# Performance work log

Hardware: AMD Instinct MI355X
Metric: run time of the kernel (lower is better)

Reference implementation:

```python
import jax, jax.numpy as jnp
import numpy as np

# GNB per-element parameters [s, beta, R, C6] indexed by atomic number Z (rows not listed stay zero)
_ROWS = {
 1:[0.2772,1.7504,3.6516,95.99], 2:[0.2425,2.087,2.1843,40.67], 3:[0.3266,2.3073,1.2711,70.21],
 4:[0.3964,2.8811,3.3497,114.51], 5:[0.3121,2.6366,2.7079,152.36], 6:[0.2455,3.0189,1.8219,184.28],
 7:[0.2743,2.9432,2.4667,482.54], 8:[0.2577,2.7407,2.365,405.57], 9:[0.2791,2.5863,1.5062,218.45],
 10:[0.2378,2.5307,1.8233,174.81], 11:[0.2592,2.5679,1.3974,181.7], 12:[0.3837,2.9613,3.3515,263.02],
 13:[0.3013,3.2377,3.0102,228.1], 14:[0.3202,3.2749,3.1629,359.43], 15:[0.3399,3.7491,3.2554,3222.12],
 16:[0.3215,3.6718,2.9539,2144.49], 17:[0.3071,3.418,3.0368,2072.46], 18:[0.2752,3.3306,2.6598,1357.42],
 19:[0.2264,2.9736,4.0877,1406.65], 20:[0.4015,3.4464,4.1275,1058.36], 21:[0.9388,4.5955,9.7282,11498.73],
 22:[0.6048,3.5334,8.5322,3361.33], 23:[0.3678,3.068,7.2344,2095.91], 24:[0.2848,2.8393,5.3605,1049.31],
 25:[0.355,3.055,3.718,966.27], 26:[0.4406,3.2628,3.6408,1571.36], 27:[0.4124,3.2622,3.4961,1183.59],
 28:[0.3139,2.749,3.5108,787.76], 29:[0.3345,2.9097,3.0537,563.93], 30:[0.3391,2.9024,3.0261,592.91],
 31:[0.3146,3.3924,3.1735,430.82], 32:[0.3327,3.2804,3.1773,812.57], 33:[0.404,3.8757,3.8357,4533.53],
 34:[0.3343,3.8562,3.1109,3440.92], 35:[0.3242,3.7067,3.2122,3859.82], 36:[0.292,3.6457,2.8263,2729.6],
 37:[0.2677,3.4421,2.412,1864.19], 38:[0.3446,3.559,1.894,1175.73], 39:[1.0038,5.7293,11.2061,32141.18],
 40:[0.6146,5.075,6.821,27655.14], 41:[0.4244,3.7156,7.2367,2864.2], 42:[0.4882,3.6853,3.901,3563.45],
 43:[0.4439,3.6987,4.0857,3266.43], 44:[0.4736,3.7826,4.045,3967.23], 45:[0.4039,3.4706,3.4813,2233.82],
 46:[0.3188,3.3433,3.0487,1393.49], 47:[0.2948,3.1186,2.7795,1315.09], 48:[0.3012,3.0853,2.8673,1311.47],
 49:[0.3351,3.5452,3.3339,1460.56], 50:[0.3134,3.2997,3.0086,1662.99], 51:[0.4081,4.1277,3.9919,8089.97],
 52:[0.3585,4.1795,3.4209,6887.05], 53:[0.3574,4.0988,3.5649,8799.32], 54:[0.3134,4.0387,3.0288,6136.5],
 55:[0.2872,3.8468,2.262,3757.31], 56:[0.3788,4.0368,1.3837,2561.18], 57:[1.0851,6.1365,12.171,66580.83],
 72:[0.5577,5.213,6.0791,27593.76], 73:[0.5308,4.7637,5.7661,15364.65], 74:[0.3926,3.6018,3.6366,2734.5],
 75:[0.5351,3.9552,4.241,4801.82], 76:[0.4701,4.0278,4.1348,5685.94], 77:[0.3661,3.6123,3.4213,2786.0],
 78:[0.3411,3.6066,3.2486,2699.79], 79:[0.3164,3.3822,2.9588,2282.6], 80:[0.3047,3.375,2.9381,2476.79],
 81:[0.2802,3.3964,2.7711,2988.7], 82:[0.2682,3.2481,2.5816,2506.63], 83:[0.3876,4.1225,3.785,8916.84],
 84:[0.3679,4.2313,3.5381,8694.22], 85:[0.368,4.2455,3.6985,11821.61], 86:[0.3195,4.1784,3.0551,8410.64],
}
_TAB = np.zeros((87, 4), np.float32)
for _z, _v in _ROWS.items():
    _TAB[_z] = _v
GNB_TABLE = jnp.asarray(_TAB)
C_SP2 = jnp.asarray(np.array([0.2808, 3.0548, 2.2348, 429.69], np.float32))
C_SP3 = jnp.asarray(np.array([0.2455, 3.0189, 1.8219, 184.28], np.float32))
N_CN2 = jnp.asarray(np.array([0.2996, 3.02, 2.6454, 720.18], np.float32))
N_CN3 = jnp.asarray(np.array([0.2743, 2.9432, 2.4667, 482.54], np.float32))

BJ_A1, BJ_A2, BJ_ALPHA = 0.4, 4.0, 14.0
CUTOFF_LR, CUTOFF_START = 10.0, 8.0  # cutoff_start = cutoff_lr - 2.0


def _poly_envelope(x):
    # PolynomialCutoff.calculate_envelope with r_max=1, p=6:
    x6 = x ** 6
    env = 1.0 - 28.0 * x6 + 48.0 * x6 * x - 21.0 * x6 * x * x
    return env * (x < 1.0)


def _gnb_forward(lengths, Z, edge_index):
    n_nodes = Z.shape[0]
    sender, receiver = edge_index[0], edge_index[1]

    # coordination numbers via scatter-add on receiver
    cn = jnp.zeros((n_nodes,), jnp.int32).at[receiver].add(1)

    # species-indexed params with CN-adaptive selection for C and N
    params = GNB_TABLE[Z]  # [N, 4]
    c_params = jnp.where((cn <= 3)[:, None], C_SP2[None, :], C_SP3[None, :])
    n_params = jnp.where((cn <= 2)[:, None], N_CN2[None, :], N_CN3[None, :])
    params = jnp.where((Z == 6)[:, None], c_params, params)
    params = jnp.where((Z == 7)[:, None], n_params, params)

    R_i = params[:, 2]
    C6_i = params[:, 3]

    # geometric-mean combination rules per edge
    C6_ij = jnp.sqrt(C6_i[sender] * C6_i[receiver])
    R_ij = jnp.sqrt(R_i[sender] * R_i[receiver])

    r = lengths
    # BJ damping: f = 1 / (1 + 6 (r/r0)^(-alpha)), r0 = a1 sqrt(R_ij) + a2
    r0 = BJ_A1 * jnp.sqrt(R_ij) + BJ_A2
    f_damp = 1.0 / (1.0 + 6.0 * (r0 / r) ** BJ_ALPHA)

    e_edge = -C6_ij / (R_ij ** 6 + r ** 6) * f_damp

    # long-range polynomial cutoff switching from 1 at cutoff_start to 0 at cutoff_lr
    x = (r - CUTOFF_START) / (CUTOFF_LR - CUTOFF_START)
    env = jnp.where(r < CUTOFF_START, 1.0, _poly_envelope(x))
    e_edge = e_edge * env

    # scatter-sum to atoms; 0.5 to split symmetric pair energy over both directions
    node_energy = jnp.zeros((n_nodes,), e_edge.dtype).at[receiver].add(0.5 * e_edge)
    return node_energy


def setup_inputs() -> dict:
    key = jax.random.key(0)
    k1, k2, k3 = jax.random.split(key, 3)
    n_nodes, n_edges = 100000, 6400000
    Z = jax.random.randint(k1, (n_nodes,), 1, 87, dtype=jnp.int32)
    edge_index = jax.random.randint(k2, (2, n_edges), 0, n_nodes, dtype=jnp.int32)
    lengths = jax.random.uniform(k3, (n_edges,), jnp.float32, 1.0, 10.5)
    return {"Z": Z, "edge_index": edge_index, "lengths": lengths}


def reference(Z, edge_index, lengths):
    return _gnb_forward(lengths, Z, edge_index)
```

## Files before the change

### kernel.cpp

```cpp
#include <hip/hip_runtime.h>


#define B2SHIFT 10
#define B2SIZE  1024
#define TILE    4096
#define SBLK    512
#define ESLICES 8
#define MAXB    128
#define AREP    4

__device__ __constant__ float2 GNB_RC6[87] = {
    {0.f, 0.f},
    {3.6516f, 95.99f},   {2.1843f, 40.67f},   {1.2711f, 70.21f},
    {3.3497f, 114.51f},  {2.7079f, 152.36f},  {1.8219f, 184.28f},
    {2.4667f, 482.54f},  {2.365f, 405.57f},   {1.5062f, 218.45f},
    {1.8233f, 174.81f},  {1.3974f, 181.7f},   {3.3515f, 263.02f},
    {3.0102f, 228.1f},   {3.1629f, 359.43f},  {3.2554f, 3222.12f},
    {2.9539f, 2144.49f}, {3.0368f, 2072.46f}, {2.6598f, 1357.42f},
    {4.0877f, 1406.65f}, {4.1275f, 1058.36f}, {9.7282f, 11498.73f},
    {8.5322f, 3361.33f}, {7.2344f, 2095.91f}, {5.3605f, 1049.31f},
    {3.718f, 966.27f},   {3.6408f, 1571.36f}, {3.4961f, 1183.59f},
    {3.5108f, 787.76f},  {3.0537f, 563.93f},  {3.0261f, 592.91f},
    {3.1735f, 430.82f},  {3.1773f, 812.57f},  {3.8357f, 4533.53f},
    {3.1109f, 3440.92f}, {3.2122f, 3859.82f}, {2.8263f, 2729.6f},
    {2.412f, 1864.19f},  {1.894f, 1175.73f},  {11.2061f, 32141.18f},
    {6.821f, 27655.14f}, {7.2367f, 2864.2f},  {3.901f, 3563.45f},
    {4.0857f, 3266.43f}, {4.045f, 3967.23f},  {3.4813f, 2233.82f},
    {3.0487f, 1393.49f}, {2.7795f, 1315.09f}, {2.8673f, 1311.47f},
    {3.3339f, 1460.56f}, {3.0086f, 1662.99f}, {3.9919f, 8089.97f},
    {3.4209f, 6887.05f}, {3.5649f, 8799.32f}, {3.0288f, 6136.5f},
    {2.262f, 3757.31f},  {1.3837f, 2561.18f}, {12.171f, 66580.83f},
    {0.f,0.f},{0.f,0.f},{0.f,0.f},{0.f,0.f},{0.f,0.f},{0.f,0.f},{0.f,0.f},
    {0.f,0.f},{0.f,0.f},{0.f,0.f},{0.f,0.f},{0.f,0.f},{0.f,0.f},{0.f,0.f},
    {6.0791f, 27593.76f}, {5.7661f, 15364.65f}, {3.6366f, 2734.5f},
    {4.241f, 4801.82f},   {4.1348f, 5685.94f},  {3.4213f, 2786.0f},
    {3.2486f, 2699.79f},  {2.9588f, 2282.6f},   {2.9381f, 2476.79f},
    {2.7711f, 2988.7f},   {2.5816f, 2506.63f},  {3.785f, 8916.84f},
    {3.5381f, 8694.22f},  {3.6985f, 11821.61f}, {3.0551f, 8410.64f},
};

__global__ void gnb_init(const int* __restrict__ Z, unsigned* __restrict__ isCN,
                         int nw, int n_nodes, int4* __restrict__ zp4, int zq,
                         int* __restrict__ zp, int zwords) {
    int stride = gridDim.x * blockDim.x;
    int t0 = blockIdx.x * blockDim.x + threadIdx.x;
    int4 z4 = make_int4(0, 0, 0, 0);
    for (int i = t0; i < zq; i += stride) zp4[i] = z4;
    for (int i = zq * 4 + t0; i < zwords; i += stride) zp[i] = 0;
    for (int w = t0; w < nw; w += stride) {
        unsigned m = 0;
        int base = w << 5;
        int lim = n_nodes - base; if (lim > 32) lim = 32;
        for (int k = 0; k < lim; ++k) {
            int z = Z[base + k];
            if (z == 6 || z == 7) m |= (1u << k);
        }
        isCN[w] = m;
    }
}

__global__ void gnb_params(const int* __restrict__ Z, const int* __restrict__ cn,
                           float2* __restrict__ P2, int n_nodes) {
    int i = blockIdx.x * blockDim.x + threadIdx.x;
    if (i >= n_nodes) return;
    int z = Z[i];
    float Rp, C6;
    if (z == 6) {
        if (cn[i] <= 3) { Rp = 2.2348f; C6 = 429.69f; }
        else            { Rp = 1.8219f; C6 = 184.28f; }
    } else if (z == 7) {
        if (cn[i] <= 2) { Rp = 2.6454f; C6 = 720.18f; }
        else            { Rp = 2.4667f; C6 = 482.54f; }
    } else {
        float2 rc = GNB_RC6[z];
        Rp = rc.x; C6 = rc.y;
    }
    P2[i] = make_float2(sqrtf(C6), sqrtf(sqrtf(Rp)));
}

__device__ __forceinline__ float gnb_energy_eval(float2 ps, float2 pr, float rlen) {
    float env;
    if (rlen < 8.0f) {
        env = 1.0f;
    } else {
        float x = (rlen - 8.0f) * 0.5f;
        float x2 = x * x;
        float x6 = x2 * x2 * x2;
        env = 1.0f - 28.0f * x6 + 48.0f * x6 * x - 21.0f * x6 * x2;
    }
    float sR  = ps.y * pr.y;
    float C6  = ps.x * pr.x;
    float Rij = sR * sR;
    float R3  = Rij * Rij * Rij;
    float R6  = R3 * R3;
    float r0  = 0.4f * sR + 4.0f;
    float t   = r0 / rlen;
    float t2 = t * t, t4 = t2 * t2, t8 = t4 * t4;
    float t14 = t8 * t4 * t2;
    float fd = 1.0f / (1.0f + 6.0f * t14);
    float rl2 = rlen * rlen;
    float r6 = rl2 * rl2 * rl2;
    return -0.5f * C6 / (R6 + r6) * fd * env;
}

__global__ void __launch_bounds__(SBLK)
gnb_scatter(const int* __restrict__ send, const int* __restrict__ recv,
            const float* __restrict__ len, const unsigned* __restrict__ isCN,
            int* __restrict__ cn,
            uint2* __restrict__ buckets, unsigned* __restrict__ cursor,
            uint4* __restrict__ ovrec, unsigned* __restrict__ ocur,
            int n_edges, unsigned cap, unsigned ocap) {
    __shared__ unsigned hist[MAXB];
    __shared__ unsigned gbase[MAXB];
    const int tid = threadIdx.x;
    const int e0  = blockIdx.x * TILE;

    if (tid < MAXB) hist[tid] = 0;
    __syncthreads();

    unsigned ss[8]; unsigned rr[8]; float ll[8];
    const bool full = (e0 + TILE <= n_edges);
    if (full) {
        int4   sv0 = *(const int4*)(send + e0 + tid * 4);
        int4   rv0 = *(const int4*)(recv + e0 + tid * 4);
        float4 lv0 = *(const float4*)(len + e0 + tid * 4);
        int4   sv1 = *(const int4*)(send + e0 + 2048 + tid * 4);
        int4   rv1 = *(const int4*)(recv + e0 + 2048 + tid * 4);
        float4 lv1 = *(const float4*)(len + e0 + 2048 + tid * 4);
        ss[0]=(unsigned)sv0.x; ss[1]=(unsigned)sv0.y; ss[2]=(unsigned)sv0.z; ss[3]=(unsigned)sv0.w;
        ss[4]=(unsigned)sv1.x; ss[5]=(unsigned)sv1.y; ss[6]=(unsigned)sv1.z; ss[7]=(unsigned)sv1.w;
        rr[0]=(unsigned)rv0.x; rr[1]=(unsigned)rv0.y; rr[2]=(unsigned)rv0.z; rr[3]=(unsigned)rv0.w;
        rr[4]=(unsigned)rv1.x; rr[5]=(unsigned)rv1.y; rr[6]=(unsigned)rv1.z; rr[7]=(unsigned)rv1.w;
        ll[0]=lv0.x; ll[1]=lv0.y; ll[2]=lv0.z; ll[3]=lv0.w;
        ll[4]=lv1.x; ll[5]=lv1.y; ll[6]=lv1.z; ll[7]=lv1.w;
    } else {
        #pragma unroll
        for (int i = 0; i < 8; ++i) {
            int e = e0 + ((i >> 2) * 2048) + tid * 4 + (i & 3);
            bool ok = (e < n_edges);
            ss[i] = ok ? (unsigned)send[e] : 0u;
            rr[i] = ok ? (unsigned)recv[e] : 0u;
            ll[i] = ok ? len[e] : 1.0e9f;
        }
    }

    #pragma unroll
    for (int i = 0; i < 8; ++i) {
        if (ll[i] < 1.0e8f && ((isCN[rr[i] >> 5] >> (rr[i] & 31)) & 1u))
            atomicAdd(&cn[rr[i]], 1);
    }

    unsigned bk[8];
    #pragma unroll
    for (int i = 0; i < 8; ++i) {
        if (ll[i] < 10.0f) {
            unsigned b   = rr[i] >> B2SHIFT;
            unsigned off = atomicAdd(&hist[b], 1u);
            bk[i] = b | (off << 7);
        } else {
            bk[i] = 0x80000000u;
        }
    }
    __syncthreads();

    if (tid < MAXB) {
        unsigned c = hist[tid];
        gbase[tid] = c ? atomicAdd(&cursor[tid], c) : 0u;
    }
    __syncthreads();

    #pragma unroll
    for (int i = 0; i < 8; ++i) {
        unsigned bo = bk[i];
        if (!(bo & 0x80000000u)) {
            unsigned b = bo & (MAXB - 1);
            unsigned g = gbase[b] + (bo >> 7);
            unsigned x = ss[i] | ((rr[i] & (B2SIZE - 1)) << 17);
            if (g < cap) {
                buckets[(size_t)b * cap + g] = make_uint2(x, __float_as_uint(ll[i]));
            } else {
                unsigned o = atomicAdd(ocur, 1u);
                if (o < ocap)
                    ovrec[o] = make_uint4(rr[i], ss[i], __float_as_uint(ll[i]), 0u);
            }
        }
    }
}

__global__ void __launch_bounds__(256)
gnb_accum(const uint2* __restrict__ buckets, const unsigned* __restrict__ cursor,
          const uint4* __restrict__ ovrec, const unsigned* __restrict__ ocur,
          const float2* __restrict__ P2, float* __restrict__ rep,
          unsigned cap, unsigned ocap, int n_nodes) {
    __shared__ float  acc[AREP][B2SIZE + 8];
    __shared__ float2 p2loc[B2SIZE];
    const int b   = blockIdx.x / ESLICES;
    const int sl  = blockIdx.x % ESLICES;
    const int tid = threadIdx.x;
    const int rp  = (tid >> 6) & (AREP - 1);

    for (int i = tid; i < AREP * (B2SIZE + 8); i += 256) acc[0][i] = 0.0f;
    for (int i = tid; i < B2SIZE; i += 256) {
        int node = (b << B2SHIFT) + i;
        p2loc[i] = (node < n_nodes) ? P2[node] : make_float2(0.f, 0.f);
    }
    __syncthreads();

    unsigned count = cursor[b];
    if (count > cap) count = cap;
    unsigned seg = (((count + ESLICES - 1) / ESLICES) + 3u) & ~3u;
    unsigned st  = (unsigned)sl * seg; if (st > count) st = count;
    unsigned en  = st + seg; if (en > count) en = count;

    const uint2* src = buckets + (size_t)b * cap;
    for (unsigned i = st + tid * 4; i < en; i += 1024) {
        if (i + 4 <= en) {
            uint4 q0 = *(const uint4*)(src + i);
            uint4 q1 = *(const uint4*)(src + i + 2);
            unsigned sx[4] = {q0.x, q0.z, q1.x, q1.z};
            unsigned lb[4] = {q0.y, q0.w, q1.y, q1.w};
            float2 ps[4];
            #pragma unroll
            for (int j = 0; j < 4; ++j) ps[j] = P2[sx[j] & 0x1FFFFu];
            #pragma unroll
            for (int j = 0; j < 4; ++j) {
                unsigned rlow = (sx[j] >> 17) & (B2SIZE - 1);
                float e = gnb_energy_eval(ps[j], p2loc[rlow], __uint_as_float(lb[j]));
                atomicAdd(&acc[rp][rlow], e);
            }
        } else {
            for (unsigned t = i; t < en; ++t) {
                uint2 rec = src[t];
                unsigned rlow = (rec.x >> 17) & (B2SIZE - 1);
                float e = gnb_energy_eval(P2[rec.x & 0x1FFFFu], p2loc[rlow],
                                          __uint_as_float(rec.y));
                atomicAdd(&acc[rp][rlow], e);
            }
        }
    }

    if (sl == 0) {
        unsigned n = *ocur; if (n > ocap) n = ocap;
        for (unsigned i = tid; i < n; i += 256) {
            uint4 rc = ovrec[i];
            if ((rc.x >> B2SHIFT) == (unsigned)b) {
                float e = gnb_energy_eval(P2[rc.y], p2loc[rc.x & (B2SIZE - 1)],
                                          __uint_as_float(rc.z));
                atomicAdd(&acc[rp][rc.x & (B2SIZE - 1)], e);
            }
        }
    }
    __syncthreads();

    float* dst = rep + (size_t)blockIdx.x * B2SIZE;
    for (int i = tid; i < B2SIZE; i += 256)
        dst[i] = (acc[0][i] + acc[1][i]) + (acc[2][i] + acc[3][i]);
}

__global__ void gnb_reduce(const float* __restrict__ rep, float* __restrict__ out,
                           int n_nodes) {
    int i = blockIdx.x * blockDim.x + threadIdx.x;
    if (i >= n_nodes) return;
    int b = i >> B2SHIFT;
    int j = i & (B2SIZE - 1);
    const float* src = rep + ((size_t)b * ESLICES) * B2SIZE + j;
    float sum = 0.0f;
    #pragma unroll
    for (int s = 0; s < ESLICES; ++s) sum += src[(size_t)s * B2SIZE];
    out[i] = sum;
}

extern "C" void kernel_launch(void* const* d_in, const int* in_sizes, int n_in,
                              void* d_out, int out_size, void* d_ws, size_t ws_size,
                              hipStream_t stream) {
    const int*   Z    = (const int*)d_in[0];
    const int*   eidx = (const int*)d_in[1];
    const float* len  = (const float*)d_in[2];
    float*       out  = (float*)d_out;

    const int n_nodes = in_sizes[0];
    const int n_edges = in_sizes[2];
    const int* send = eidx;
    const int* recv = eidx + n_edges;

    const int NB2 = (n_nodes + B2SIZE - 1) >> B2SHIFT;
    const int nw  = (n_nodes + 31) >> 5;
    const int nwp = (nw + 7) & ~7;

    char* ws = (char*)d_ws;
    unsigned* cursor = (unsigned*)ws;
    unsigned* ocur   = (unsigned*)(ws + MAXB * 4);
    int*      cn     = (int*)(ws + (MAXB + 8) * 4);
    float2*   P2     = (float2*)(ws + ((size_t)n_nodes + MAXB + 8) * 4);
    unsigned* isCN   = (unsigned*)(ws + ((size_t)3 * n_nodes + MAXB + 8) * 4);
    float*    rep    = (float*)((char*)isCN + (size_t)nwp * 4);
    size_t rep_w     = (size_t)NB2 * ESLICES * B2SIZE;
    char*     tail   = (char*)rep + rep_w * 4;

    size_t fixed_words = (size_t)3 * n_nodes + MAXB + 8 + nwp + rep_w;
    size_t total_words = ws_size / 4;
    size_t avail = total_words > fixed_words ? total_words - fixed_words : 0;
    size_t ovw = avail / 64;
    unsigned ocap = (unsigned)(ovw / 4);
    size_t capw = (avail - ovw) / (size_t)NB2;
    long cap = (long)((capw / 2) & ~(size_t)3);
    if (cap > n_edges) cap = (n_edges + 3) & ~3;
    if (cap < 0) cap = 0;
    uint4* ovrec   = (uint4*)tail;
    uint2* buckets = (uint2*)(tail + (size_t)ocap * 16);

    const int B = 256;
    int node_blocks = (n_nodes + B - 1) / B;
    int scat_blocks = (n_edges + TILE - 1) / TILE;
    int zero_words  = n_nodes + MAXB + 8;
    int zq = zero_words / 4;

    gnb_init<<<256, B, 0, stream>>>(Z, isCN, nw, n_nodes, (int4*)ws, zq,
                                    (int*)ws, zero_words);
    gnb_scatter<<<scat_blocks, SBLK, 0, stream>>>(send, recv, len, isCN, cn,
                                                  buckets, cursor, ovrec, ocur,
                                                  n_edges, (unsigned)cap, ocap);
    gnb_params<<<node_blocks, B, 0, stream>>>(Z, cn, P2, n_nodes);
    gnb_accum<<<NB2 * ESLICES, B, 0, stream>>>(buckets, cursor, ovrec, ocur,
                                               P2, rep, (unsigned)cap, ocap,
                                               n_nodes);
    gnb_reduce<<<node_blocks, B, 0, stream>>>(rep, out, n_nodes);
}
```

Baseline: 200.0 us.

## Fuse pipeline into single cooperative persistent kernel with work-stealing phases

Replaces the five separate launches (init, scatter, params, accum, reduce) with one cooperative kernel. The kernel separates the phases with grid-wide syncs and uses atomic work-stealing counters to hand out edge tiles and accumulation units. The scatter tile shrinks to 2048 edges per 256-thread block, and accumulation slices per bucket rise from 8 to 32 for better load balance. The aim is to remove launch gaps and tail imbalance. In exchange it pays for grid syncs and reads a larger partial-sum buffer in the final reduction. The original multi-kernel path is kept as a fallback if the cooperative launch fails.

```diff
diff --git a/kernel.cpp b/kernel.cpp
--- a/kernel.cpp
+++ b/kernel.cpp
@@ -1,13 +1,19 @@
 #include <hip/hip_runtime.h>
+#include <hip/hip_cooperative_groups.h>
+
+namespace cg = cooperative_groups;
 
 
 #define B2SHIFT 10
 #define B2SIZE  1024
-#define TILE    4096
-#define SBLK    512
-#define ESLICES 8
 #define MAXB    128
+#define ESLICES 32
+#define BLK     256
+#define EPT     8
+#define STILE   (BLK * EPT)
 #define AREP    4
+#define FTILE   4096
+#define FSBLK   512
 
 __device__ __constant__ float2 GNB_RC6[87] = {
     {0.f, 0.f},
@@ -39,45 +45,6 @@
     {3.5381f, 8694.22f},  {3.6985f, 11821.61f}, {3.0551f, 8410.64f},
 };
 
-__global__ void gnb_init(const int* __restrict__ Z, unsigned* __restrict__ isCN,
-                         int nw, int n_nodes, int4* __restrict__ zp4, int zq,
-                         int* __restrict__ zp, int zwords) {
-    int stride = gridDim.x * blockDim.x;
-    int t0 = blockIdx.x * blockDim.x + threadIdx.x;
-    int4 z4 = make_int4(0, 0, 0, 0);
-    for (int i = t0; i < zq; i += stride) zp4[i] = z4;
-    for (int i = zq * 4 + t0; i < zwords; i += stride) zp[i] = 0;
-    for (int w = t0; w < nw; w += stride) {
-        unsigned m = 0;
-        int base = w << 5;
-        int lim = n_nodes - base; if (lim > 32) lim = 32;
-        for (int k = 0; k < lim; ++k) {
-            int z = Z[base + k];
-            if (z == 6 || z == 7) m |= (1u << k);
-        }
-        isCN[w] = m;
-    }
-}
-
-__global__ void gnb_params(const int* __restrict__ Z, const int* __restrict__ cn,
-                           float2* __restrict__ P2, int n_nodes) {
-    int i = blockIdx.x * blockDim.x + threadIdx.x;
-    if (i >= n_nodes) return;
-    int z = Z[i];
-    float Rp, C6;
-    if (z == 6) {
-        if (cn[i] <= 3) { Rp = 2.2348f; C6 = 429.69f; }
-        else            { Rp = 1.8219f; C6 = 184.28f; }
-    } else if (z == 7) {
-        if (cn[i] <= 2) { Rp = 2.6454f; C6 = 720.18f; }
-        else            { Rp = 2.4667f; C6 = 482.54f; }
-    } else {
-        float2 rc = GNB_RC6[z];
-        Rp = rc.x; C6 = rc.y;
-    }
-    P2[i] = make_float2(sqrtf(C6), sqrtf(sqrtf(Rp)));
-}
-
 __device__ __forceinline__ float gnb_energy_eval(float2 ps, float2 pr, float rlen) {
     float env;
     if (rlen < 8.0f) {
@@ -103,23 +70,277 @@
     return -0.5f * C6 / (R6 + r6) * fd * env;
 }
 
-__global__ void __launch_bounds__(SBLK)
-gnb_scatter(const int* __restrict__ send, const int* __restrict__ recv,
-            const float* __restrict__ len, const unsigned* __restrict__ isCN,
-            int* __restrict__ cn,
-            uint2* __restrict__ buckets, unsigned* __restrict__ cursor,
-            uint4* __restrict__ ovrec, unsigned* __restrict__ ocur,
-            int n_edges, unsigned cap, unsigned ocap) {
+__device__ __forceinline__ void params_one(const int* Z, const int* cn,
+                                           float2* P2, int i) {
+    int z = Z[i];
+    float Rp, C6;
+    if (z == 6) {
+        if (cn[i] <= 3) { Rp = 2.2348f; C6 = 429.69f; }
+        else            { Rp = 1.8219f; C6 = 184.28f; }
+    } else if (z == 7) {
+        if (cn[i] <= 2) { Rp = 2.6454f; C6 = 720.18f; }
+        else            { Rp = 2.4667f; C6 = 482.54f; }
+    } else {
+        float2 rc = GNB_RC6[z];
+        Rp = rc.x; C6 = rc.y;
+    }
+    P2[i] = make_float2(sqrtf(C6), sqrtf(sqrtf(Rp)));
+}
+
+__global__ void __launch_bounds__(BLK)
+gnb_fused(const int* __restrict__ Z, const int* __restrict__ send,
+          const int* __restrict__ recv, const float* __restrict__ len,
+          float* __restrict__ out,
+          unsigned* __restrict__ cursor, unsigned* __restrict__ cntrs,
+          int* __restrict__ cn, float2* __restrict__ P2,
+          unsigned* __restrict__ isCN, float* __restrict__ rep,
+          uint4* __restrict__ ovrec, uint2* __restrict__ buckets,
+          int n_nodes, int n_edges, unsigned cap, unsigned ocap,
+          int nw, int NB2, int ntiles, int nunits) {
+    cg::grid_group grid = cg::this_grid();
+    __shared__ union {
+        struct { unsigned hist[MAXB]; unsigned gbase[MAXB]; } s;
+        struct { float acc[AREP][B2SIZE + 8]; float2 p2loc[B2SIZE]; } a;
+    } sh;
+    __shared__ unsigned steal;
+    const int tid = threadIdx.x;
+    const int gtid = blockIdx.x * BLK + tid;
+    const int gstride = gridDim.x * BLK;
+    unsigned* ocur = cntrs + 0;
+    unsigned* scur = cntrs + 1;
+    unsigned* ucur = cntrs + 2;
+
+    {
+        int zwords = MAXB + 8 + n_nodes;
+        int zq = zwords >> 2;
+        int4* zp4 = (int4*)cursor;
+        int4 z4 = make_int4(0, 0, 0, 0);
+        for (int i = gtid; i < zq; i += gstride) zp4[i] = z4;
+        for (int i = (zq << 2) + gtid; i < zwords; i += gstride)
+            ((int*)cursor)[i] = 0;
+        int nal = (n_nodes + 63) & ~63;
+        for (int i = gtid; i < nal; i += gstride) {
+            bool pred = false;
+            if (i < n_nodes) { int z = Z[i]; pred = (z == 6) | (z == 7); }
+            unsigned long long m = __ballot(pred);
+            if ((tid & 63) == 0) {
+                int w = i >> 5;
+                if (w < nw)     isCN[w]     = (unsigned)m;
+                if (w + 1 < nw) isCN[w + 1] = (unsigned)(m >> 32);
+            }
+        }
+    }
+    grid.sync();
+
+    for (;;) {
+        if (tid == 0) steal = atomicAdd(scur, 1u);
+        __syncthreads();
+        unsigned t = steal;
+        if (t >= (unsigned)ntiles) break;
+        if (tid < MAXB) sh.s.hist[tid] = 0;
+        __syncthreads();
+
+        const int e0 = (int)t * STILE;
+        unsigned ss[EPT]; unsigned rr[EPT]; float ll[EPT];
+        const bool full = (e0 + STILE <= n_edges);
+        if (full) {
+            int4   sv0 = *(const int4*)(send + e0 + tid * 4);
+            int4   rv0 = *(const int4*)(recv + e0 + tid * 4);
+            float4 lv0 = *(const float4*)(len + e0 + tid * 4);
+            int4   sv1 = *(const int4*)(send + e0 + 1024 + tid * 4);
+            int4   rv1 = *(const int4*)(recv + e0 + 1024 + tid * 4);
+            float4 lv1 = *(const float4*)(len + e0 + 1024 + tid * 4);
+            ss[0]=(unsigned)sv0.x; ss[1]=(unsigned)sv0.y; ss[2]=(unsigned)sv0.z; ss[3]=(unsigned)sv0.w;
+            ss[4]=(unsigned)sv1.x; ss[5]=(unsigned)sv1.y; ss[6]=(unsigned)sv1.z; ss[7]=(unsigned)sv1.w;
+            rr[0]=(unsigned)rv0.x; rr[1]=(unsigned)rv0.y; rr[2]=(unsigned)rv0.z; rr[3]=(unsigned)rv0.w;
+            rr[4]=(unsigned)rv1.x; rr[5]=(unsigned)rv1.y; rr[6]=(unsigned)rv1.z; rr[7]=(unsigned)rv1.w;
+            ll[0]=lv0.x; ll[1]=lv0.y; ll[2]=lv0.z; ll[3]=lv0.w;
+            ll[4]=lv1.x; ll[5]=lv1.y; ll[6]=lv1.z; ll[7]=lv1.w;
+        } else {
+            #pragma unroll
+            for (int i = 0; i < EPT; ++i) {
+                int e = e0 + ((i >> 2) * 1024) + tid * 4 + (i & 3);
+                bool ok = (e < n_edges);
+                ss[i] = ok ? (unsigned)send[e] : 0u;
+                rr[i] = ok ? (unsigned)recv[e] : 0u;
+                ll[i] = ok ? len[e] : 1.0e9f;
+            }
+        }
+
+        #pragma unroll
+        for (int i = 0; i < EPT; ++i) {
+            if (ll[i] < 1.0e8f && ((isCN[rr[i] >> 5] >> (rr[i] & 31)) & 1u))
+                atomicAdd(&cn[rr[i]], 1);
+        }
+
+        unsigned bk[EPT];
+        #pragma unroll
+        for (int i = 0; i < EPT; ++i) {
+            if (ll[i] < 10.0f) {
+                unsigned b   = rr[i] >> B2SHIFT;
+                unsigned off = atomicAdd(&sh.s.hist[b], 1u);
+                bk[i] = b | (off << 7);
+            } else {
+                bk[i] = 0x80000000u;
+            }
+        }
+        __syncthreads();
+
+        if (tid < MAXB) {
+            unsigned c = sh.s.hist[tid];
+            sh.s.gbase[tid] = c ? atomicAdd(&cursor[tid], c) : 0u;
+        }
+        __syncthreads();
+
+        #pragma unroll
+        for (int i = 0; i < EPT; ++i) {
+            unsigned bo = bk[i];
+            if (!(bo & 0x80000000u)) {
+                unsigned b = bo & (MAXB - 1);
+                unsigned g = sh.s.gbase[b] + (bo >> 7);
+                unsigned x = ss[i] | ((rr[i] & (B2SIZE - 1)) << 17);
+                if (g < cap) {
+                    buckets[(size_t)b * cap + g] =
+                        make_uint2(x, __float_as_uint(ll[i]));
+                } else {
+                    unsigned o = atomicAdd(ocur, 1u);
+                    if (o < ocap)
+                        ovrec[o] = make_uint4(rr[i], ss[i],
+                                              __float_as_uint(ll[i]), 0u);
+                }
+            }
+        }
+    }
+    grid.sync();
+
+    for (int i = gtid; i < n_nodes; i += gstride) params_one(Z, cn, P2, i);
+    grid.sync();
+
+    for (;;) {
+        if (tid == 0) steal = atomicAdd(ucur, 1u);
+        __syncthreads();
+        unsigned u = steal;
+        if (u >= (unsigned)nunits) break;
+        const int b  = (int)(u >> 5);
+        const int sl = (int)(u & (ESLICES - 1));
+        const int rp = (tid >> 6) & (AREP - 1);
+
+        float* accf = &sh.a.acc[0][0];
+        for (int i = tid; i < AREP * (B2SIZE + 8); i += BLK) accf[i] = 0.0f;
+        for (int i = tid; i < B2SIZE; i += BLK) {
+            int node = (b << B2SHIFT) + i;
+            sh.a.p2loc[i] = (node < n_nodes) ? P2[node] : make_float2(0.f, 0.f);
+        }
+        __syncthreads();
+
+        unsigned count = cursor[b];
+        if (count > cap) count = cap;
+        unsigned seg = (((count + ESLICES - 1) / ESLICES) + 3u) & ~3u;
+        unsigned st  = (unsigned)sl * seg; if (st > count) st = count;
+        unsigned en  = st + seg; if (en > count) en = count;
+
+        const uint2* src = buckets + (size_t)b * cap;
+        for (unsigned i = st + tid * 4; i < en; i += BLK * 4) {
+            if (i + 4 <= en) {
+                uint4 q0 = *(const uint4*)(src + i);
+                uint4 q1 = *(const uint4*)(src + i + 2);
+                unsigned sx[4] = {q0.x, q0.z, q1.x, q1.z};
+                unsigned lb[4] = {q0.y, q0.w, q1.y, q1.w};
+                float2 ps[4];
+                #pragma unroll
+                for (int j = 0; j < 4; ++j) ps[j] = P2[sx[j] & 0x1FFFFu];
+                #pragma unroll
+                for (int j = 0; j < 4; ++j) {
+                    unsigned rlow = (sx[j] >> 17) & (B2SIZE - 1);
+                    float e = gnb_energy_eval(ps[j], sh.a.p2loc[rlow],
+                                              __uint_as_float(lb[j]));
+                    atomicAdd(&sh.a.acc[rp][rlow], e);
+                }
+            } else {
+                for (unsigned q = i; q < en; ++q) {
+                    uint2 rec = src[q];
+                    unsigned rlow = (rec.x >> 17) & (B2SIZE - 1);
+                    float e = gnb_energy_eval(P2[rec.x & 0x1FFFFu],
+                                              sh.a.p2loc[rlow],
+                                              __uint_as_float(rec.y));
+                    atomicAdd(&sh.a.acc[rp][rlow], e);
+                }
+            }
+        }
+
+        if (sl == 0) {
+            unsigned n = *ocur; if (n > ocap) n = ocap;
+            for (unsigned i = tid; i < n; i += BLK) {
+                uint4 rc = ovrec[i];
+                if ((rc.x >> B2SHIFT) == (unsigned)b) {
+                    float e = gnb_energy_eval(P2[rc.y],
+                                              sh.a.p2loc[rc.x & (B2SIZE - 1)],
+                                              __uint_as_float(rc.z));
+                    atomicAdd(&sh.a.acc[rp][rc.x & (B2SIZE - 1)], e);
+                }
+            }
+        }
+        __syncthreads();
+
+        float* dst = rep + (size_t)u * B2SIZE;
+        for (int i = tid; i < B2SIZE; i += BLK)
+            dst[i] = (sh.a.acc[0][i] + sh.a.acc[1][i]) +
+                     (sh.a.acc[2][i] + sh.a.acc[3][i]);
+    }
+    grid.sync();
+
+    for (int i = gtid; i < n_nodes; i += gstride) {
+        int b = i >> B2SHIFT;
+        int j = i & (B2SIZE - 1);
+        const float* src = rep + ((size_t)b * ESLICES) * B2SIZE + j;
+        float s = 0.0f;
+        #pragma unroll
+        for (int k = 0; k < ESLICES; ++k) s += src[(size_t)k * B2SIZE];
+        out[i] = s;
+    }
+}
+
+__global__ void fb_init(const int* __restrict__ Z, unsigned* __restrict__ isCN,
+                        int nw, int n_nodes, int4* __restrict__ zp4, int zq,
+                        int* __restrict__ zp, int zwords) {
+    int stride = gridDim.x * blockDim.x;
+    int t0 = blockIdx.x * blockDim.x + threadIdx.x;
+    int4 z4 = make_int4(0, 0, 0, 0);
+    for (int i = t0; i < zq; i += stride) zp4[i] = z4;
+    for (int i = zq * 4 + t0; i < zwords; i += stride) zp[i] = 0;
+    for (int w = t0; w < nw; w += stride) {
+        unsigned m = 0;
+        int base = w << 5;
+        int lim = n_nodes - base; if (lim > 32) lim = 32;
+        for (int k = 0; k < lim; ++k) {
+            int z = Z[base + k];
+            if (z == 6 || z == 7) m |= (1u << k);
+        }
+        isCN[w] = m;
+    }
+}
+
+__global__ void fb_params(const int* __restrict__ Z, const int* __restrict__ cn,
+                          float2* __restrict__ P2, int n_nodes) {
+    int i = blockIdx.x * blockDim.x + threadIdx.x;
+    if (i < n_nodes) params_one(Z, cn, P2, i);
+}
+
+__global__ void __launch_bounds__(FSBLK)
+fb_scatter(const int* __restrict__ send, const int* __restrict__ recv,
+           const float* __restrict__ len, const unsigned* __restrict__ isCN,
+           int* __restrict__ cn,
+           uint2* __restrict__ buckets, unsigned* __restrict__ cursor,
+           uint4* __restrict__ ovrec, unsigned* __restrict__ ocur,
+           int n_edges, unsigned cap, unsigned ocap) {
     __shared__ unsigned hist[MAXB];
     __shared__ unsigned gbase[MAXB];
     const int tid = threadIdx.x;
-    const int e0  = blockIdx.x * TILE;
-
+    const int e0  = blockIdx.x * FTILE;
     if (tid < MAXB) hist[tid] = 0;
     __syncthreads();
-
     unsigned ss[8]; unsigned rr[8]; float ll[8];
-    const bool full = (e0 + TILE <= n_edges);
+    const bool full = (e0 + FTILE <= n_edges);
     if (full) {
         int4   sv0 = *(const int4*)(send + e0 + tid * 4);
         int4   rv0 = *(const int4*)(recv + e0 + tid * 4);
@@ -143,13 +364,11 @@
             ll[i] = ok ? len[e] : 1.0e9f;
         }
     }
-
     #pragma unroll
     for (int i = 0; i < 8; ++i) {
         if (ll[i] < 1.0e8f && ((isCN[rr[i] >> 5] >> (rr[i] & 31)) & 1u))
             atomicAdd(&cn[rr[i]], 1);
     }
-
     unsigned bk[8];
     #pragma unroll
     for (int i = 0; i < 8; ++i) {
@@ -162,13 +381,11 @@
         }
     }
     __syncthreads();
-
     if (tid < MAXB) {
         unsigned c = hist[tid];
         gbase[tid] = c ? atomicAdd(&cursor[tid], c) : 0u;
     }
     __syncthreads();
-
     #pragma unroll
     for (int i = 0; i < 8; ++i) {
         unsigned bo = bk[i];
@@ -187,33 +404,30 @@
     }
 }
 
-__global__ void __launch_bounds__(256)
-gnb_accum(const uint2* __restrict__ buckets, const unsigned* __restrict__ cursor,
-          const uint4* __restrict__ ovrec, const unsigned* __restrict__ ocur,
-          const float2* __restrict__ P2, float* __restrict__ rep,
-          unsigned cap, unsigned ocap, int n_nodes) {
+__global__ void __launch_bounds__(BLK)
+fb_accum(const uint2* __restrict__ buckets, const unsigned* __restrict__ cursor,
+         const uint4* __restrict__ ovrec, const unsigned* __restrict__ ocur,
+         const float2* __restrict__ P2, float* __restrict__ rep,
+         unsigned cap, unsigned ocap, int n_nodes) {
     __shared__ float  acc[AREP][B2SIZE + 8];
     __shared__ float2 p2loc[B2SIZE];
     const int b   = blockIdx.x / ESLICES;
     const int sl  = blockIdx.x % ESLICES;
     const int tid = threadIdx.x;
     const int rp  = (tid >> 6) & (AREP - 1);
-
-    for (int i = tid; i < AREP * (B2SIZE + 8); i += 256) acc[0][i] = 0.0f;
-    for (int i = tid; i < B2SIZE; i += 256) {
+    for (int i = tid; i < AREP * (B2SIZE + 8); i += BLK) acc[0][i] = 0.0f;
+    for (int i = tid; i < B2SIZE; i += BLK) {
         int node = (b << B2SHIFT) + i;
         p2loc[i] = (node < n_nodes) ? P2[node] : make_float2(0.f, 0.f);
     }
     __syncthreads();
-
     unsigned count = cursor[b];
     if (count > cap) count = cap;
     unsigned seg = (((count + ESLICES - 1) / ESLICES) + 3u) & ~3u;
     unsigned st  = (unsigned)sl * seg; if (st > count) st = count;
     unsigned en  = st + seg; if (en > count) en = count;
-
     const uint2* src = buckets + (size_t)b * cap;
-    for (unsigned i = st + tid * 4; i < en; i += 1024) {
+    for (unsigned i = st + tid * 4; i < en; i += BLK * 4) {
         if (i + 4 <= en) {
             uint4 q0 = *(const uint4*)(src + i);
             uint4 q1 = *(const uint4*)(src + i + 2);
@@ -229,8 +443,8 @@
                 atomicAdd(&acc[rp][rlow], e);
             }
         } else {
-            for (unsigned t = i; t < en; ++t) {
-                uint2 rec = src[t];
+            for (unsigned q = i; q < en; ++q) {
+                uint2 rec = src[q];
                 unsigned rlow = (rec.x >> 17) & (B2SIZE - 1);
                 float e = gnb_energy_eval(P2[rec.x & 0x1FFFFu], p2loc[rlow],
                                           __uint_as_float(rec.y));
@@ -238,10 +452,9 @@
             }
         }
     }
-
     if (sl == 0) {
         unsigned n = *ocur; if (n > ocap) n = ocap;
-        for (unsigned i = tid; i < n; i += 256) {
+        for (unsigned i = tid; i < n; i += BLK) {
             uint4 rc = ovrec[i];
             if ((rc.x >> B2SHIFT) == (unsigned)b) {
                 float e = gnb_energy_eval(P2[rc.y], p2loc[rc.x & (B2SIZE - 1)],
@@ -251,14 +464,13 @@
         }
     }
     __syncthreads();
-
     float* dst = rep + (size_t)blockIdx.x * B2SIZE;
-    for (int i = tid; i < B2SIZE; i += 256)
+    for (int i = tid; i < B2SIZE; i += BLK)
         dst[i] = (acc[0][i] + acc[1][i]) + (acc[2][i] + acc[3][i]);
 }
 
-__global__ void gnb_reduce(const float* __restrict__ rep, float* __restrict__ out,
-                           int n_nodes) {
+__global__ void fb_reduce(const float* __restrict__ rep, float* __restrict__ out,
+                          int n_nodes) {
     int i = blockIdx.x * blockDim.x + threadIdx.x;
     if (i >= n_nodes) return;
     int b = i >> B2SHIFT;
@@ -289,7 +501,7 @@
 
     char* ws = (char*)d_ws;
     unsigned* cursor = (unsigned*)ws;
-    unsigned* ocur   = (unsigned*)(ws + MAXB * 4);
+    unsigned* cntrs  = (unsigned*)(ws + MAXB * 4);
     int*      cn     = (int*)(ws + (MAXB + 8) * 4);
     float2*   P2     = (float2*)(ws + ((size_t)n_nodes + MAXB + 8) * 4);
     unsigned* isCN   = (unsigned*)(ws + ((size_t)3 * n_nodes + MAXB + 8) * 4);
@@ -309,20 +521,51 @@
     uint4* ovrec   = (uint4*)tail;
     uint2* buckets = (uint2*)(tail + (size_t)ocap * 16);
 
-    const int B = 256;
-    int node_blocks = (n_nodes + B - 1) / B;
-    int scat_blocks = (n_edges + TILE - 1) / TILE;
-    int zero_words  = n_nodes + MAXB + 8;
-    int zq = zero_words / 4;
-
-    gnb_init<<<256, B, 0, stream>>>(Z, isCN, nw, n_nodes, (int4*)ws, zq,
-                                    (int*)ws, zero_words);
-    gnb_scatter<<<scat_blocks, SBLK, 0, stream>>>(send, recv, len, isCN, cn,
-                                                  buckets, cursor, ovrec, ocur,
-                                                  n_edges, (unsigned)cap, ocap);
-    gnb_params<<<node_blocks, B, 0, stream>>>(Z, cn, P2, n_nodes);
-    gnb_accum<<<NB2 * ESLICES, B, 0, stream>>>(buckets, cursor, ovrec, ocur,
-                                               P2, rep, (unsigned)cap, ocap,
-                                               n_nodes);
-    gnb_reduce<<<node_blocks, B, 0, stream>>>(rep, out, n_nodes);
-}
+    int ntiles = (n_edges + STILE - 1) / STILE;
+    int nunits = NB2 * ESLICES;
+    unsigned capu = (unsigned)cap;
+
+    static int s_grid = -2;
+    if (s_grid == -2) {
+        s_grid = -1;
+        hipDeviceProp_t prop;
+        if (hipGetDeviceProperties(&prop, 0) == hipSuccess) {
+            int mab = 0;
+            if (hipOccupancyMaxActiveBlocksPerMultiprocessor(
+                    &mab, gnb_fused, BLK, 0) == hipSuccess && mab > 0)
+                s_grid = prop.multiProcessorCount * mab;
+        }
+    }
+
+    bool coop_ok = false;
+    if (s_grid > 0) {
+        int nn = n_nodes, ne = n_edges, nwv = nw, nb2 = NB2, nt = ntiles,
+            nu = nunits;
+        void* args[] = {
+            (void*)&Z, (void*)&send, (void*)&recv, (void*)&len, (void*)&out,
+            (void*)&cursor, (void*)&cntrs, (void*)&cn, (void*)&P2,
+            (void*)&isCN, (void*)&rep, (void*)&ovrec, (void*)&buckets,
+            (void*)&nn, (void*)&ne, (void*)&capu, (void*)&ocap,
+            (void*)&nwv, (void*)&nb2, (void*)&nt, (void*)&nu };
+        coop_ok = hipLaunchCooperativeKernel((const void*)gnb_fused,
+                                             dim3(s_grid), dim3(BLK),
+                                             args, 0, stream) == hipSuccess;
+    }
+
+    if (!coop_ok) {
+        const int B = 256;
+        int node_blocks = (n_nodes + B - 1) / B;
+        int scat_blocks = (n_edges + FTILE - 1) / FTILE;
+        int zero_words  = n_nodes + MAXB + 8;
+        int zq = zero_words / 4;
+        fb_init<<<256, B, 0, stream>>>(Z, isCN, nw, n_nodes, (int4*)ws, zq,
+                                       (int*)ws, zero_words);
+        fb_scatter<<<scat_blocks, FSBLK, 0, stream>>>(send, recv, len, isCN, cn,
+                                                      buckets, cursor, ovrec,
+                                                      cntrs, n_edges, capu, ocap);
+        fb_params<<<node_blocks, B, 0, stream>>>(Z, cn, P2, n_nodes);
+        fb_accum<<<nunits, BLK, 0, stream>>>(buckets, cursor, ovrec, cntrs,
+                                             P2, rep, capu, ocap, n_nodes);
+        fb_reduce<<<node_blocks, B, 0, stream>>>(rep, out, n_nodes);
+    }
+}
```

Measured after the change: 476.8 us. +138.4%, slower.

## Fuse slice reduction into accumulation via last-block counter, double slices

Applied to the files above, without the earlier changes.

The accumulation kernel now splits each node bucket into 16 slices instead of 8 and keeps two shared-memory replicas instead of four. The separate reduce kernel is removed. Each block bumps a per-bucket done counter, and the last block of a bucket sums the partial results and writes the output. This drops one kernel launch and gives more blocks for parallelism, at the cost of more partial-buffer traffic, more shared-atomic contention per replica, and a threadfence-based serialized tail.

```diff
diff --git a/kernel.cpp b/kernel.cpp
--- a/kernel.cpp
+++ b/kernel.cpp
@@ -5,9 +5,10 @@
 #define B2SIZE  1024
 #define TILE    4096
 #define SBLK    512
-#define ESLICES 8
+#define ESLICES 16
 #define MAXB    128
-#define AREP    4
+#define AREP    2
+#define BLK     256
 
 __device__ __constant__ float2 GNB_RC6[87] = {
     {0.f, 0.f},
@@ -187,20 +188,22 @@
     }
 }
 
-__global__ void __launch_bounds__(256)
+__global__ void __launch_bounds__(BLK)
 gnb_accum(const uint2* __restrict__ buckets, const unsigned* __restrict__ cursor,
           const uint4* __restrict__ ovrec, const unsigned* __restrict__ ocur,
           const float2* __restrict__ P2, float* __restrict__ rep,
+          unsigned* __restrict__ done, float* __restrict__ out,
           unsigned cap, unsigned ocap, int n_nodes) {
     __shared__ float  acc[AREP][B2SIZE + 8];
     __shared__ float2 p2loc[B2SIZE];
-    const int b   = blockIdx.x / ESLICES;
-    const int sl  = blockIdx.x % ESLICES;
+    __shared__ unsigned lastflag;
+    const int b   = blockIdx.x >> 4;
+    const int sl  = blockIdx.x & (ESLICES - 1);
     const int tid = threadIdx.x;
     const int rp  = (tid >> 6) & (AREP - 1);
 
-    for (int i = tid; i < AREP * (B2SIZE + 8); i += 256) acc[0][i] = 0.0f;
-    for (int i = tid; i < B2SIZE; i += 256) {
+    for (int i = tid; i < AREP * (B2SIZE + 8); i += BLK) acc[0][i] = 0.0f;
+    for (int i = tid; i < B2SIZE; i += BLK) {
         int node = (b << B2SHIFT) + i;
         p2loc[i] = (node < n_nodes) ? P2[node] : make_float2(0.f, 0.f);
     }
@@ -213,7 +216,7 @@
     unsigned en  = st + seg; if (en > count) en = count;
 
     const uint2* src = buckets + (size_t)b * cap;
-    for (unsigned i = st + tid * 4; i < en; i += 1024) {
+    for (unsigned i = st + tid * 4; i < en; i += BLK * 4) {
         if (i + 4 <= en) {
             uint4 q0 = *(const uint4*)(src + i);
             uint4 q1 = *(const uint4*)(src + i + 2);
@@ -229,8 +232,8 @@
                 atomicAdd(&acc[rp][rlow], e);
             }
         } else {
-            for (unsigned t = i; t < en; ++t) {
-                uint2 rec = src[t];
+            for (unsigned q = i; q < en; ++q) {
+                uint2 rec = src[q];
                 unsigned rlow = (rec.x >> 17) & (B2SIZE - 1);
                 float e = gnb_energy_eval(P2[rec.x & 0x1FFFFu], p2loc[rlow],
                                           __uint_as_float(rec.y));
@@ -241,7 +244,7 @@
 
     if (sl == 0) {
         unsigned n = *ocur; if (n > ocap) n = ocap;
-        for (unsigned i = tid; i < n; i += 256) {
+        for (unsigned i = tid; i < n; i += BLK) {
             uint4 rc = ovrec[i];
             if ((rc.x >> B2SHIFT) == (unsigned)b) {
                 float e = gnb_energy_eval(P2[rc.y], p2loc[rc.x & (B2SIZE - 1)],
@@ -253,21 +256,26 @@
     __syncthreads();
 
     float* dst = rep + (size_t)blockIdx.x * B2SIZE;
-    for (int i = tid; i < B2SIZE; i += 256)
-        dst[i] = (acc[0][i] + acc[1][i]) + (acc[2][i] + acc[3][i]);
-}
-
-__global__ void gnb_reduce(const float* __restrict__ rep, float* __restrict__ out,
-                           int n_nodes) {
-    int i = blockIdx.x * blockDim.x + threadIdx.x;
-    if (i >= n_nodes) return;
-    int b = i >> B2SHIFT;
-    int j = i & (B2SIZE - 1);
-    const float* src = rep + ((size_t)b * ESLICES) * B2SIZE + j;
-    float sum = 0.0f;
-    #pragma unroll
-    for (int s = 0; s < ESLICES; ++s) sum += src[(size_t)s * B2SIZE];
-    out[i] = sum;
+    for (int i = tid; i < B2SIZE; i += BLK)
+        dst[i] = acc[0][i] + acc[1][i];
+
+    __threadfence();
+    if (tid == 0) lastflag = atomicAdd(&done[b], 1u);
+    __syncthreads();
+    if (lastflag == ESLICES - 1) {
+        __threadfence();
+        const float* srcr = rep + ((size_t)b * ESLICES) * B2SIZE;
+        for (int i = tid; i < B2SIZE; i += BLK) {
+            int node = (b << B2SHIFT) + i;
+            if (node < n_nodes) {
+                float s = 0.0f;
+                #pragma unroll
+                for (int k = 0; k < ESLICES; ++k)
+                    s += srcr[(size_t)k * B2SIZE + i];
+                out[node] = s;
+            }
+        }
+    }
 }
 
 extern "C" void kernel_launch(void* const* d_in, const int* in_sizes, int n_in,
@@ -286,18 +294,22 @@
     const int NB2 = (n_nodes + B2SIZE - 1) >> B2SHIFT;
     const int nw  = (n_nodes + 31) >> 5;
     const int nwp = (nw + 7) & ~7;
+    const int cnw = (n_nodes + 3) & ~3;
 
     char* ws = (char*)d_ws;
     unsigned* cursor = (unsigned*)ws;
-    unsigned* ocur   = (unsigned*)(ws + MAXB * 4);
-    int*      cn     = (int*)(ws + (MAXB + 8) * 4);
-    float2*   P2     = (float2*)(ws + ((size_t)n_nodes + MAXB + 8) * 4);
-    unsigned* isCN   = (unsigned*)(ws + ((size_t)3 * n_nodes + MAXB + 8) * 4);
+    unsigned* done   = (unsigned*)(ws + MAXB * 4);
+    unsigned* cntrs  = (unsigned*)(ws + 2 * MAXB * 4);
+    int*      cn     = (int*)(ws + (2 * MAXB + 8) * 4);
+    float2*   P2     = (float2*)(ws + ((size_t)cnw + 2 * MAXB + 8) * 4);
+    unsigned* isCN   = (unsigned*)(ws + ((size_t)cnw + 2 * (size_t)n_nodes
+                                         + 2 * MAXB + 8) * 4);
     float*    rep    = (float*)((char*)isCN + (size_t)nwp * 4);
     size_t rep_w     = (size_t)NB2 * ESLICES * B2SIZE;
     char*     tail   = (char*)rep + rep_w * 4;
 
-    size_t fixed_words = (size_t)3 * n_nodes + MAXB + 8 + nwp + rep_w;
+    size_t fixed_words = (size_t)cnw + 2 * (size_t)n_nodes + 2 * MAXB + 8
+                         + nwp + rep_w;
     size_t total_words = ws_size / 4;
     size_t avail = total_words > fixed_words ? total_words - fixed_words : 0;
     size_t ovw = avail / 64;
@@ -312,17 +324,17 @@
     const int B = 256;
     int node_blocks = (n_nodes + B - 1) / B;
     int scat_blocks = (n_edges + TILE - 1) / TILE;
-    int zero_words  = n_nodes + MAXB + 8;
+    int nunits      = NB2 * ESLICES;
+    int zero_words  = cnw + 2 * MAXB + 8;
     int zq = zero_words / 4;
 
     gnb_init<<<256, B, 0, stream>>>(Z, isCN, nw, n_nodes, (int4*)ws, zq,
                                     (int*)ws, zero_words);
     gnb_scatter<<<scat_blocks, SBLK, 0, stream>>>(send, recv, len, isCN, cn,
-                                                  buckets, cursor, ovrec, ocur,
+                                                  buckets, cursor, ovrec, cntrs,
                                                   n_edges, (unsigned)cap, ocap);
     gnb_params<<<node_blocks, B, 0, stream>>>(Z, cn, P2, n_nodes);
-    gnb_accum<<<NB2 * ESLICES, B, 0, stream>>>(buckets, cursor, ovrec, ocur,
-                                               P2, rep, (unsigned)cap, ocap,
-                                               n_nodes);
-    gnb_reduce<<<node_blocks, B, 0, stream>>>(rep, out, n_nodes);
-}
+    gnb_accum<<<nunits, BLK, 0, stream>>>(buckets, cursor, ovrec, cntrs,
+                                          P2, rep, done, out,
+                                          (unsigned)cap, ocap, n_nodes);
+}
```

Result: slower. 385.0 us (+92.5%).
